# Kernel tuning notes

Hardware: AMD Instinct MI355X
Metric: run time of the kernel (lower is better)

Reference implementation:

```python
import jax, jax.numpy as jnp
import numpy as np

B, L, D, H, NL, V, W = 4, 2048, 512, 8, 4, 258, 8
HD = D // H


def setup_inputs() -> dict:
    key = jax.random.key(0)
    ks = jax.random.split(key, 12)
    s = 0.02
    x = jax.random.randint(ks[0], (B, L), 0, V, dtype=jnp.int32)
    patch_lengths = jnp.full((B, 256), W, dtype=jnp.int32)  # sum over patches == L
    emb = jax.random.normal(ks[1], (V, D), jnp.float32) * s
    ent_w = jax.random.normal(ks[2], (D, 1), jnp.float32) * s
    ent_b = jnp.zeros((D,), jnp.float32)
    qkv_w = jax.random.normal(ks[3], (NL, 3 * D, D), jnp.float32) * s
    qkv_b = jnp.zeros((NL, 3 * D), jnp.float32)
    ao_w = jax.random.normal(ks[4], (NL, D, D), jnp.float32) * s
    ao_b = jnp.zeros((NL, D), jnp.float32)
    ln1_s = jnp.ones((NL, D), jnp.float32)
    ln1_b = jnp.zeros((NL, D), jnp.float32)
    ln2_s = jnp.ones((NL, D), jnp.float32)
    ln2_b = jnp.zeros((NL, D), jnp.float32)
    ff1_w = jax.random.normal(ks[5], (NL, 4 * D, D), jnp.float32) * s
    ff1_b = jnp.zeros((NL, 4 * D), jnp.float32)
    ff2_w = jax.random.normal(ks[6], (NL, D, 4 * D), jnp.float32) * s
    ff2_b = jnp.zeros((NL, D), jnp.float32)
    out_w = jax.random.normal(ks[7], (V, D), jnp.float32) * s
    return {"emb": emb, "ent_w": ent_w, "ent_b": ent_b, "qkv_w": qkv_w,
            "qkv_b": qkv_b, "ao_w": ao_w, "ao_b": ao_b, "ln1_s": ln1_s,
            "ln1_b": ln1_b, "ln2_s": ln2_s, "ln2_b": ln2_b, "ff1_w": ff1_w,
            "ff1_b": ff1_b, "ff2_w": ff2_w, "ff2_b": ff2_b, "out_w": out_w,
            "x": x, "patch_lengths": patch_lengths}


def _layernorm(h, scale, bias, eps=1e-5):
    mu = jnp.mean(h, axis=-1, keepdims=True)
    var = jnp.mean(jnp.square(h - mu), axis=-1, keepdims=True)
    return (h - mu) * jax.lax.rsqrt(var + eps) * scale + bias


def _entropy_features(x, dtype):
    # fused sliding-window histogram via one-hot cumsum (replaces per-window bincount loop)
    onehot = jax.nn.one_hot(x, 256, dtype=dtype)            # [B, L, 256]
    c = jnp.cumsum(onehot, axis=1)
    cpad = jnp.concatenate([jnp.zeros_like(c[:, :1]), c], axis=1)
    counts = cpad[:, W:] - cpad[:, :-W]                     # [B, L-W+1, 256]
    p = counts / W
    ent = -jnp.sum(p * jnp.log2(p + 1e-10), axis=-1)        # zero-count terms contribute exactly 0
    full = jnp.zeros(x.shape, dtype).at[:, :x.shape[1] - W + 1].set(ent)
    return full[..., None]                                  # [B, L, 1]


def _block(h, p):
    qkv_w, qkv_b, ao_w, ao_b, l1s, l1b, l2s, l2b, f1w, f1b, f2w, f2b = p
    g = _layernorm(h, l1s, l1b)
    qkv = g @ qkv_w.T + qkv_b                                # [B, L, 3D]
    q, k, v = jnp.split(qkv, 3, axis=-1)
    q = q.reshape(B, L, H, HD)
    k = k.reshape(B, L, H, HD)
    v = v.reshape(B, L, H, HD)
    scores = jnp.einsum('blhd,bmhd->bhlm', q, k) / np.sqrt(HD).astype(h.dtype)
    attn = jax.nn.softmax(scores, axis=-1)
    o = jnp.einsum('bhlm,bmhd->blhd', attn, v).reshape(B, L, D)
    h = h + o @ ao_w.T + ao_b
    g = _layernorm(h, l2s, l2b)
    g = jax.nn.gelu(g @ f1w.T + f1b, approximate=False) @ f2w.T + f2b
    return h + g, None


def reference(emb, ent_w, ent_b, qkv_w, qkv_b, ao_w, ao_b, ln1_s, ln1_b,
              ln2_s, ln2_b, ff1_w, ff1_b, ff2_w, ff2_b, out_w, x, patch_lengths):
    tok = emb[x]                                             # [B, L, D]
    ent = _entropy_features(x, tok.dtype)                    # [B, L, 1]
    ent_emb = ent * ent_w[:, 0] + ent_b                      # Linear(1, D)
    h = tok + ent_emb
    h, _ = jax.lax.scan(_block, h,
                        (qkv_w, qkv_b, ao_w, ao_b, ln1_s, ln1_b,
                         ln2_s, ln2_b, ff1_w, ff1_b, ff2_w, ff2_b))
    # NOTE: the original module's global_transformer/patch-pool branch does not
    # feed the returned logits (dead code); logits come from the local stream h.
    logits = h @ out_w.T                                     # [B, L, V]
    return logits
```

## Files before the change

### kernel.cpp

```cpp
#include <hip/hip_runtime.h>
#include <hip/hip_bf16.h>
#include <math.h>

#define BB 4
#define LL 2048
#define DD 512
#define HH 8
#define NLAYER 4
#define VV 258
#define WW 8
#define HDIM 64
#define MM (BB * LL)
#define VPAD 384

#define C8 0.18033688f

typedef __attribute__((ext_vector_type(8))) short short8v;
typedef __attribute__((ext_vector_type(4))) float float4v;

typedef __attribute__((address_space(3))) unsigned int lds_u32;
typedef const __attribute__((address_space(1))) unsigned int glb_u32;

__device__ __forceinline__ unsigned short f2bf(float x) {
    unsigned int u = __float_as_uint(x);
    unsigned int r = (u + 0x7fffu + ((u >> 16) & 1u)) >> 16;
    return (unsigned short)r;
}
__device__ __forceinline__ float bf2f(unsigned short u) {
    return __uint_as_float((unsigned)u << 16);
}

__device__ __forceinline__ unsigned lds_addr(const void* p) {
    return (unsigned)(size_t)(__attribute__((address_space(3))) const void*)p;
}

#define E0 (NLAYER * 3 * DD * DD)
#define E1 (E0 + NLAYER * DD * DD)
#define E2 (E1 + NLAYER * 4 * DD * DD)
#define E3 (E2 + NLAYER * 4 * DD * DD)
#define E4 (E3 + VPAD * DD)

__global__ __launch_bounds__(256)
void cvt_all_kernel(const float* __restrict__ qkv_w, const float* __restrict__ ao_w,
                    const float* __restrict__ ff1_w, const float* __restrict__ ff2_w,
                    const float* __restrict__ out_w, unsigned short* __restrict__ dst)
{
    int i = (blockIdx.x * 256 + threadIdx.x) * 4;
    float4 v;
    if (i < E0)      v = *reinterpret_cast<const float4*>(qkv_w + i);
    else if (i < E1) v = *reinterpret_cast<const float4*>(ao_w + (i - E0));
    else if (i < E2) v = *reinterpret_cast<const float4*>(ff1_w + (i - E1));
    else if (i < E3) v = *reinterpret_cast<const float4*>(ff2_w + (i - E2));
    else {
        int idx = i - E3;
        if ((idx >> 9) < VV) v = *reinterpret_cast<const float4*>(out_w + idx);
        else                 v = (float4){0.f, 0.f, 0.f, 0.f};
    }
    uint2 pk;
    pk.x = (unsigned)f2bf(v.x) | ((unsigned)f2bf(v.y) << 16);
    pk.y = (unsigned)f2bf(v.z) | ((unsigned)f2bf(v.w) << 16);
    *reinterpret_cast<uint2*>(dst + i) = pk;
}

__global__ __launch_bounds__(256)
void embed_ln_kernel(const int* __restrict__ x,
                     const float* __restrict__ emb,
                     const float* __restrict__ ent_w,
                     const float* __restrict__ ent_b,
                     const float* __restrict__ ln_s,
                     const float* __restrict__ ln_b,
                     unsigned short* __restrict__ h,
                     unsigned short* __restrict__ g)
{
    int w = threadIdx.x >> 6, lane = threadIdx.x & 63;
    int row = blockIdx.x * 4 + w;
    int b = row / LL, l = row % LL;

    float ent = 0.f;
    if (l <= LL - WW) {
        int win[WW];
        #pragma unroll
        for (int i = 0; i < WW; i++) win[i] = x[b * LL + l + i];
        float s = 0.f;
        #pragma unroll
        for (int i = 0; i < WW; i++) {
            if (win[i] < 256) {
                int c = 0;
                #pragma unroll
                for (int j = 0; j < WW; j++) c += (win[j] == win[i]) ? 1 : 0;
                s += log2f((float)c * 0.125f + 1e-10f);
            }
        }
        ent = -s * 0.125f;
    }

    int tok = x[row];
    const float* erow = emb + (size_t)tok * DD + lane * 8;
    float v[8], ew[8], eb[8];
    *reinterpret_cast<float4*>(v)      = *reinterpret_cast<const float4*>(erow);
    *reinterpret_cast<float4*>(v + 4)  = *reinterpret_cast<const float4*>(erow + 4);
    *reinterpret_cast<float4*>(ew)     = *reinterpret_cast<const float4*>(ent_w + lane * 8);
    *reinterpret_cast<float4*>(ew + 4) = *reinterpret_cast<const float4*>(ent_w + lane * 8 + 4);
    *reinterpret_cast<float4*>(eb)     = *reinterpret_cast<const float4*>(ent_b + lane * 8);
    *reinterpret_cast<float4*>(eb + 4) = *reinterpret_cast<const float4*>(ent_b + lane * 8 + 4);

    float sum = 0.f, sq = 0.f;
    #pragma unroll
    for (int i = 0; i < 8; i++) {
        v[i] = v[i] + ent * ew[i] + eb[i];
        sum += v[i]; sq += v[i] * v[i];
    }
    unsigned int hpk[4];
    #pragma unroll
    for (int i = 0; i < 4; i++)
        hpk[i] = (unsigned)f2bf(v[2*i]) | ((unsigned)f2bf(v[2*i+1]) << 16);
    *reinterpret_cast<uint4*>(h + (size_t)row * DD + lane * 8) =
        *reinterpret_cast<const uint4*>(hpk);

    #pragma unroll
    for (int off = 32; off > 0; off >>= 1) {
        sum += __shfl_xor(sum, off);
        sq  += __shfl_xor(sq, off);
    }
    float mu = sum * (1.f / DD);
    float var = sq * (1.f / DD) - mu * mu;
    float rstd = rsqrtf(var + 1e-5f);

    float s8[8], bi[8];
    *reinterpret_cast<float4*>(s8)     = *reinterpret_cast<const float4*>(ln_s + lane * 8);
    *reinterpret_cast<float4*>(s8 + 4) = *reinterpret_cast<const float4*>(ln_s + lane * 8 + 4);
    *reinterpret_cast<float4*>(bi)     = *reinterpret_cast<const float4*>(ln_b + lane * 8);
    *reinterpret_cast<float4*>(bi + 4) = *reinterpret_cast<const float4*>(ln_b + lane * 8 + 4);

    unsigned int pk[4];
    #pragma unroll
    for (int i = 0; i < 4; i++) {
        unsigned short lo = f2bf((v[2*i]   - mu) * rstd * s8[2*i]   + bi[2*i]);
        unsigned short hi = f2bf((v[2*i+1] - mu) * rstd * s8[2*i+1] + bi[2*i+1]);
        pk[i] = (unsigned)lo | ((unsigned)hi << 16);
    }
    *reinterpret_cast<uint4*>(g + (size_t)row * DD + lane * 8) =
        *reinterpret_cast<const uint4*>(pk);
}

__global__ __launch_bounds__(256)
void ln_kernel(const unsigned short* __restrict__ h,
               const float* __restrict__ scale,
               const float* __restrict__ bias,
               unsigned short* __restrict__ g)
{
    int w = threadIdx.x >> 6, lane = threadIdx.x & 63;
    int row = blockIdx.x * 4 + w;

    uint4 raw = *reinterpret_cast<const uint4*>(h + (size_t)row * DD + lane * 8);
    const unsigned* rw = reinterpret_cast<const unsigned*>(&raw);
    float v[8];
    #pragma unroll
    for (int i = 0; i < 4; i++) {
        v[2*i]   = __uint_as_float(rw[i] << 16);
        v[2*i+1] = __uint_as_float(rw[i] & 0xffff0000u);
    }

    float sum = 0.f, sq = 0.f;
    #pragma unroll
    for (int i = 0; i < 8; i++) { sum += v[i]; sq += v[i] * v[i]; }
    #pragma unroll
    for (int off = 32; off > 0; off >>= 1) {
        sum += __shfl_xor(sum, off);
        sq  += __shfl_xor(sq, off);
    }
    float mu = sum * (1.f / DD);
    float var = sq * (1.f / DD) - mu * mu;
    float rstd = rsqrtf(var + 1e-5f);

    float s[8], bi[8];
    *reinterpret_cast<float4*>(s)      = *reinterpret_cast<const float4*>(scale + lane * 8);
    *reinterpret_cast<float4*>(s + 4)  = *reinterpret_cast<const float4*>(scale + lane * 8 + 4);
    *reinterpret_cast<float4*>(bi)     = *reinterpret_cast<const float4*>(bias + lane * 8);
    *reinterpret_cast<float4*>(bi + 4) = *reinterpret_cast<const float4*>(bias + lane * 8 + 4);

    unsigned int pk[4];
    #pragma unroll
    for (int i = 0; i < 4; i++) {
        unsigned short lo = f2bf((v[2*i]   - mu) * rstd * s[2*i]   + bi[2*i]);
        unsigned short hi = f2bf((v[2*i+1] - mu) * rstd * s[2*i+1] + bi[2*i+1]);
        pk[i] = (unsigned)lo | ((unsigned)hi << 16);
    }
    *reinterpret_cast<uint4*>(g + (size_t)row * DD + lane * 8) =
        *reinterpret_cast<const uint4*>(pk);
}

template<bool HAS_BIAS, bool GELU, bool RESID, int OMODE, int MT>
__global__ __launch_bounds__(MT * 2)
void gemm_mfma(const unsigned short* __restrict__ A,
               const unsigned short* __restrict__ W,
               const float* __restrict__ bias,
               const unsigned short* __restrict__ resid,
               void* __restrict__ Cv,
               int Nn, int Kk)
{
    constexpr int NW = MT / 32;
    constexpr int BLOADS = 512 / MT;
    constexpr int VMN = 4 + BLOADS;

    __shared__ unsigned short As[2][MT * 64];
    __shared__ unsigned short Bs[2][128 * 64];

    int t = threadIdx.x;
    int w = t >> 6, lane = t & 63;
    int wr = (MT == 128) ? (w >> 1) : 0;
    int wc = (MT == 128) ? (w & 1) : w;
    int l15 = lane & 15, l4 = lane >> 4;
    int m0 = blockIdx.y * MT, n0 = blockIdx.x * 128;

    int lrow = lane >> 3;
    int segp = (lane & 7) ^ lrow;

    float4v acc[4][4];
    #pragma unroll
    for (int i = 0; i < 4; i++)
        #pragma unroll
        for (int j = 0; j < 4; j++)
            acc[i][j] = (float4v){0.f, 0.f, 0.f, 0.f};

    #define STAGE(buf, k0) do {                                                   \
        _Pragma("unroll")                                                         \
        for (int i_ = 0; i_ < 4; i_++) {                                          \
            int r_ = i_ * (NW * 8) + w * 8 + lrow;                                \
            __builtin_amdgcn_global_load_lds(                                     \
                (glb_u32*)(A + (size_t)(m0 + r_) * Kk + (k0) + segp * 8),         \
                (lds_u32*)(As[buf] + i_ * (NW * 512) + w * 512), 16, 0, 0);       \
        }                                                                         \
        _Pragma("unroll")                                                         \
        for (int i_ = 0; i_ < BLOADS; i_++) {                                     \
            int r_ = i_ * (NW * 8) + w * 8 + lrow;                                \
            __builtin_amdgcn_global_load_lds(                                     \
                (glb_u32*)(W + (size_t)(n0 + r_) * Kk + (k0) + segp * 8),         \
                (lds_u32*)(Bs[buf] + i_ * (NW * 512) + w * 512), 16, 0, 0);       \
        } } while (0)

    int nk = Kk >> 6;
    STAGE(0, 0);
    for (int kt = 0; kt < nk; kt++) {
        int cur = kt & 1;
        if (kt + 1 < nk) {
            STAGE(cur ^ 1, (kt + 1) << 6);
            __builtin_amdgcn_sched_barrier(0);
            if constexpr (VMN == 8)  asm volatile("s_waitcnt vmcnt(8)");
            else                     asm volatile("s_waitcnt vmcnt(12)");
            __builtin_amdgcn_sched_barrier(0);
        } else {
            __builtin_amdgcn_sched_barrier(0);
            asm volatile("s_waitcnt vmcnt(0)");
            __builtin_amdgcn_sched_barrier(0);
        }
        __builtin_amdgcn_s_barrier();

        const char* asb = (const char*)As[cur];
        const char* bsb = (const char*)Bs[cur];
        #pragma unroll
        for (int kc = 0; kc < 2; kc++) {
            short8v af[4], bfr[4];
            #pragma unroll
            for (int mf = 0; mf < 4; mf++) {
                int row = wr * 64 + mf * 16 + l15;
                int off = (row * 128 + kc * 64 + l4 * 16) ^ ((row & 7) << 4);
                af[mf] = *reinterpret_cast<const short8v*>(asb + off);
            }
            #pragma unroll
            for (int nf = 0; nf < 4; nf++) {
                int row = wc * 64 + nf * 16 + l15;
                int off = (row * 128 + kc * 64 + l4 * 16) ^ ((row & 7) << 4);
                bfr[nf] = *reinterpret_cast<const short8v*>(bsb + off);
            }
            #pragma unroll
            for (int mf = 0; mf < 4; mf++)
                #pragma unroll
                for (int nf = 0; nf < 4; nf++)
                    acc[mf][nf] = __builtin_amdgcn_mfma_f32_16x16x32_bf16(
                        af[mf], bfr[nf], acc[mf][nf], 0, 0, 0);
        }
        __builtin_amdgcn_s_barrier();
    }
    #undef STAGE

    #pragma unroll
    for (int mf = 0; mf < 4; mf++)
        #pragma unroll
        for (int nf = 0; nf < 4; nf++)
            #pragma unroll
            for (int r = 0; r < 4; r++) {
                int m = m0 + wr * 64 + mf * 16 + l4 * 4 + r;
                int n = n0 + wc * 64 + nf * 16 + l15;
                if (n < Nn) {
                    float v = acc[mf][nf][r];
                    if (HAS_BIAS) v += bias[n];
                    if (GELU)     v = 0.5f * v * (1.f + erff(v * 0.70710678118654752f));
                    if (RESID)    v += bf2f(resid[(size_t)m * Nn + n]);
                    if (OMODE == 1)
                        ((unsigned short*)Cv)[(size_t)m * Nn + n] = f2bf(v);
                    else
                        ((float*)Cv)[(size_t)m * Nn + n] = v;
                }
            }
}

__global__ __launch_bounds__(512, 2)
void attn_mfma(const unsigned short* __restrict__ qkv, unsigned short* __restrict__ o)
{
    __shared__ unsigned short Kl[2][64 * 64];
    __shared__ unsigned short Vs[2][64 * 64];
    __shared__ unsigned short Pl[8 * 16 * 64];
    __shared__ float Scl[8][16];

    int t = threadIdx.x, w = t >> 6, lane = t & 63;
    int l15 = lane & 15, l4 = lane >> 4;

    int flat = blockIdx.x;
    int swz = (flat & 7) * 64 + (flat >> 3);
    int qt = swz & 15, hh = (swz >> 4) & 7, b = swz >> 7;

    int q0 = qt * 128 + w * 16;
    const int RS = 3 * DD;

    short8v qf[2];
    #pragma unroll
    for (int dh = 0; dh < 2; dh++) {
        size_t addr = (size_t)(b * LL + q0 + l15) * RS + hh * HDIM + dh * 32 + l4 * 8;
        qf[dh] = *reinterpret_cast<const short8v*>(qkv + addr);
    }

    float4v o_acc[4];
    #pragma unroll
    for (int dt = 0; dt < 4; dt++) o_acc[dt] = (float4v){0.f, 0.f, 0.f, 0.f};
    float l_run = 0.f;

    char* pbase = (char*)Pl + w * 2048;

    int lrow8 = lane >> 3;
    int ksegp = (lane & 7) ^ lrow8;
    int vrow = ((t >> 5) << 2) | ((t >> 1) & 3);
    int vseg = (((t >> 3) & 3) << 1) | (t & 1);
    const unsigned short* kgl = qkv + (size_t)(b * LL + w * 8 + lrow8) * RS
                              + hh * HDIM + DD + ksegp * 8;
    const unsigned short* vgl = qkv + (size_t)(b * LL + vrow) * RS
                              + hh * HDIM + 2 * DD + vseg * 8;
    const int step = 64 * RS;

    #define ASTAGE(buf) do {                                                      \
        __builtin_amdgcn_global_load_lds((glb_u32*)kgl,                           \
            (lds_u32*)(Kl[buf] + w * 512), 16, 0, 0);                             \
        __builtin_amdgcn_global_load_lds((glb_u32*)vgl,                           \
            (lds_u32*)(Vs[buf] + w * 512), 16, 0, 0);                             \
        kgl += step; vgl += step; } while (0)

    unsigned vtrbase = lds_addr(Vs) + ((lane >> 4) << 10)
                     + (((lane >> 2) & 3) << 5) + ((lane & 3) << 3);
    unsigned pswz = (unsigned)((l15 & 7) << 4);
    unsigned pa0 = lds_addr(pbase) + ((unsigned)(l15 * 128 + l4 * 16) ^ pswz);
    unsigned pa1 = lds_addr(pbase) + ((unsigned)(l15 * 128 + 64 + l4 * 16) ^ pswz);

    ASTAGE(0);
    asm volatile("s_waitcnt vmcnt(0)");
    __syncthreads();

    for (int kb = 0; kb < LL / 64; kb++) {
        int cur = kb & 1;
        if (kb + 1 < LL / 64) ASTAGE(cur ^ 1);

        const char* klc = (const char*)Kl[cur];
        unsigned vb = vtrbase + cur * 8192;

        float4v s_acc[4];
        __builtin_amdgcn_s_setprio(1);
        #pragma unroll
        for (int nt = 0; nt < 4; nt++) {
            s_acc[nt] = (float4v){0.f, 0.f, 0.f, 0.f};
            #pragma unroll
            for (int dh = 0; dh < 2; dh++) {
                int row = nt * 16 + l15;
                int off = (row * 128 + dh * 64 + l4 * 16) ^ ((row & 7) << 4);
                short8v kf = *reinterpret_cast<const short8v*>(klc + off);
                s_acc[nt] = __builtin_amdgcn_mfma_f32_16x16x32_bf16(kf, qf[dh], s_acc[nt], 0, 0, 0);
            }
        }
        __builtin_amdgcn_s_setprio(0);

        float ps = 0.f;
        #pragma unroll
        for (int nt = 0; nt < 4; nt++) {
            float p0 = __builtin_amdgcn_exp2f(s_acc[nt][0] * C8);
            float p1 = __builtin_amdgcn_exp2f(s_acc[nt][1] * C8);
            float p2 = __builtin_amdgcn_exp2f(s_acc[nt][2] * C8);
            float p3 = __builtin_amdgcn_exp2f(s_acc[nt][3] * C8);
            ps += (p0 + p1) + (p2 + p3);
            unsigned int pk0, pk1;
            asm("v_cvt_pk_bf16_f32 %0, %1, %2" : "=v"(pk0) : "v"(p0), "v"(p1));
            asm("v_cvt_pk_bf16_f32 %0, %1, %2" : "=v"(pk1) : "v"(p2), "v"(p3));
            uint2 pk; pk.x = pk0; pk.y = pk1;
            int off = (l15 * 128 + nt * 32 + l4 * 8) ^ ((l15 & 7) << 4);
            *reinterpret_cast<uint2*>(pbase + off) = pk;
        }
        l_run += ps;

        short8v pf0, pf1;
        asm volatile("ds_read_b128 %0, %1" : "=v"(pf0) : "v"(pa0) : "memory");
        asm volatile("ds_read_b128 %0, %1" : "=v"(pf1) : "v"(pa1) : "memory");
        unsigned long long a0, a1, a2, a3, a4, a5, a6, a7;
        unsigned long long b0, b1, b2, b3, b4, b5, b6, b7;
        unsigned ab0 = vb, ab1 = vb + 4096;
        asm volatile("ds_read_b64_tr_b16 %0, %1" : "=v"(a0) : "v"(ab0));
        asm volatile("ds_read_b64_tr_b16 %0, %1" : "=v"(a1) : "v"(ab0 + 512));
        asm volatile("ds_read_b64_tr_b16 %0, %1" : "=v"(a2) : "v"(ab0 + 128));
        asm volatile("ds_read_b64_tr_b16 %0, %1" : "=v"(a3) : "v"(ab0 + 640));
        asm volatile("ds_read_b64_tr_b16 %0, %1" : "=v"(a4) : "v"(ab0 + 256));
        asm volatile("ds_read_b64_tr_b16 %0, %1" : "=v"(a5) : "v"(ab0 + 768));
        asm volatile("ds_read_b64_tr_b16 %0, %1" : "=v"(a6) : "v"(ab0 + 384));
        asm volatile("ds_read_b64_tr_b16 %0, %1" : "=v"(a7) : "v"(ab0 + 896));
        asm volatile("ds_read_b64_tr_b16 %0, %1" : "=v"(b0) : "v"(ab1));
        asm volatile("ds_read_b64_tr_b16 %0, %1" : "=v"(b1) : "v"(ab1 + 512));
        asm volatile("ds_read_b64_tr_b16 %0, %1" : "=v"(b2) : "v"(ab1 + 128));
        asm volatile("ds_read_b64_tr_b16 %0, %1" : "=v"(b3) : "v"(ab1 + 640));
        asm volatile("ds_read_b64_tr_b16 %0, %1" : "=v"(b4) : "v"(ab1 + 256));
        asm volatile("ds_read_b64_tr_b16 %0, %1" : "=v"(b5) : "v"(ab1 + 768));
        asm volatile("ds_read_b64_tr_b16 %0, %1" : "=v"(b6) : "v"(ab1 + 384));
        asm volatile("ds_read_b64_tr_b16 %0, %1" : "=v"(b7) : "v"(ab1 + 896));
        union { unsigned long long q[2]; short8v v; } u0, u1, u2, u3;
        __builtin_amdgcn_s_setprio(1);
        asm volatile("s_waitcnt lgkmcnt(12)");
        __builtin_amdgcn_sched_barrier(0);
        u0.q[0] = a0; u0.q[1] = a1;
        u1.q[0] = a2; u1.q[1] = a3;
        o_acc[0] = __builtin_amdgcn_mfma_f32_16x16x32_bf16(pf0, u0.v, o_acc[0], 0, 0, 0);
        o_acc[1] = __builtin_amdgcn_mfma_f32_16x16x32_bf16(pf0, u1.v, o_acc[1], 0, 0, 0);
        asm volatile("s_waitcnt lgkmcnt(8)");
        __builtin_amdgcn_sched_barrier(0);
        u2.q[0] = a4; u2.q[1] = a5;
        u3.q[0] = a6; u3.q[1] = a7;
        o_acc[2] = __builtin_amdgcn_mfma_f32_16x16x32_bf16(pf0, u2.v, o_acc[2], 0, 0, 0);
        o_acc[3] = __builtin_amdgcn_mfma_f32_16x16x32_bf16(pf0, u3.v, o_acc[3], 0, 0, 0);
        asm volatile("s_waitcnt lgkmcnt(4)");
        __builtin_amdgcn_sched_barrier(0);
        u0.q[0] = b0; u0.q[1] = b1;
        u1.q[0] = b2; u1.q[1] = b3;
        o_acc[0] = __builtin_amdgcn_mfma_f32_16x16x32_bf16(pf1, u0.v, o_acc[0], 0, 0, 0);
        o_acc[1] = __builtin_amdgcn_mfma_f32_16x16x32_bf16(pf1, u1.v, o_acc[1], 0, 0, 0);
        asm volatile("s_waitcnt lgkmcnt(0)");
        __builtin_amdgcn_sched_barrier(0);
        u2.q[0] = b4; u2.q[1] = b5;
        u3.q[0] = b6; u3.q[1] = b7;
        o_acc[2] = __builtin_amdgcn_mfma_f32_16x16x32_bf16(pf1, u2.v, o_acc[2], 0, 0, 0);
        o_acc[3] = __builtin_amdgcn_mfma_f32_16x16x32_bf16(pf1, u3.v, o_acc[3], 0, 0, 0);
        __builtin_amdgcn_s_setprio(0);

        asm volatile("s_waitcnt vmcnt(0)");
        __syncthreads();
    }
    #undef ASTAGE

    float lt = l_run;
    lt += __shfl_xor(lt, 16);
    lt += __shfl_xor(lt, 32);
    if (l4 == 0) Scl[w][l15] = 1.f / lt;
    float4 iv = *reinterpret_cast<const float4*>(&Scl[w][l4 * 4]);
    float invs[4] = {iv.x, iv.y, iv.z, iv.w};
    #pragma unroll
    for (int r = 0; r < 4; r++) {
        int qg = q0 + l4 * 4 + r;
        #pragma unroll
        for (int dt = 0; dt < 4; dt++) {
            o[(size_t)(b * LL + qg) * DD + hh * HDIM + dt * 16 + l15] =
                f2bf(o_acc[dt][r] * invs[r]);
        }
    }
}

extern "C" void kernel_launch(void* const* d_in, const int* in_sizes, int n_in,
                              void* d_out, int out_size, void* d_ws, size_t ws_size,
                              hipStream_t stream)
{
    const float* emb    = (const float*)d_in[0];
    const float* ent_w  = (const float*)d_in[1];
    const float* ent_b  = (const float*)d_in[2];
    const float* qkv_w  = (const float*)d_in[3];
    const float* qkv_b  = (const float*)d_in[4];
    const float* ao_w   = (const float*)d_in[5];
    const float* ao_b   = (const float*)d_in[6];
    const float* ln1_s  = (const float*)d_in[7];
    const float* ln1_b  = (const float*)d_in[8];
    const float* ln2_s  = (const float*)d_in[9];
    const float* ln2_b  = (const float*)d_in[10];
    const float* ff1_w  = (const float*)d_in[11];
    const float* ff1_b  = (const float*)d_in[12];
    const float* ff2_w  = (const float*)d_in[13];
    const float* ff2_b  = (const float*)d_in[14];
    const float* out_w  = (const float*)d_in[15];
    const int*   x      = (const int*)d_in[16];

    float* out = (float*)d_out;

    const int NQW = NLAYER * 3 * DD * DD;
    const int NAW = NLAYER * DD * DD;
    const int NF1 = NLAYER * 4 * DD * DD;
    const int NF2 = NLAYER * DD * 4 * DD;

    char* p = (char*)d_ws;
    unsigned short* wq  = (unsigned short*)p; p += (size_t)NQW * 2;
    unsigned short* wa  = (unsigned short*)p; p += (size_t)NAW * 2;
    unsigned short* w1  = (unsigned short*)p; p += (size_t)NF1 * 2;
    unsigned short* w2  = (unsigned short*)p; p += (size_t)NF2 * 2;
    unsigned short* wob = (unsigned short*)p; p += (size_t)VPAD * DD * 2;
    unsigned short* h   = (unsigned short*)p; p += (size_t)MM * DD * 2;
    unsigned short* gb  = (unsigned short*)p; p += (size_t)MM * DD * 2;
    unsigned short* ob  = (unsigned short*)p; p += (size_t)MM * DD * 2;
    unsigned short* bb  = (unsigned short*)p; p += (size_t)MM * 4 * DD * 2;

    dim3 blk(256);

    cvt_all_kernel<<<E4 / 1024, blk, 0, stream>>>(qkv_w, ao_w, ff1_w, ff2_w, out_w, wq);

    embed_ln_kernel<<<MM / 4, blk, 0, stream>>>(x, emb, ent_w, ent_b,
                                                ln1_s, ln1_b, h, gb);

    for (int layer = 0; layer < NLAYER; layer++) {
        const unsigned short* qw = wq + (size_t)layer * 3 * DD * DD;
        const unsigned short* aw = wa + (size_t)layer * DD * DD;
        const unsigned short* f1 = w1 + (size_t)layer * 4 * DD * DD;
        const unsigned short* f2 = w2 + (size_t)layer * DD * 4 * DD;
        const float* qb  = qkv_b + (size_t)layer * 3 * DD;
        const float* ab  = ao_b  + (size_t)layer * DD;
        const float* l1s = ln1_s + (size_t)layer * DD;
        const float* l1b = ln1_b + (size_t)layer * DD;
        const float* l2s = ln2_s + (size_t)layer * DD;
        const float* l2b = ln2_b + (size_t)layer * DD;
        const float* f1b = ff1_b + (size_t)layer * 4 * DD;
        const float* f2b = ff2_b + (size_t)layer * DD;

        if (layer > 0)
            ln_kernel<<<MM / 4, blk, 0, stream>>>(h, l1s, l1b, gb);

        {
            dim3 grid((3 * DD) / 128, MM / 128);
            gemm_mfma<true, false, false, 1, 128><<<grid, 256, 0, stream>>>(
                gb, qw, qb, nullptr, bb, 3 * DD, DD);
        }

        attn_mfma<<<512, 512, 0, stream>>>(bb, ob);

        {
            dim3 grid(DD / 128, MM / 64);
            gemm_mfma<true, false, true, 1, 64><<<grid, 128, 0, stream>>>(
                ob, aw, ab, h, h, DD, DD);
        }

        ln_kernel<<<MM / 4, blk, 0, stream>>>(h, l2s, l2b, gb);

        {
            dim3 grid((4 * DD) / 128, MM / 128);
            gemm_mfma<true, true, false, 1, 128><<<grid, 256, 0, stream>>>(
                gb, f1, f1b, nullptr, bb, 4 * DD, DD);
        }

        {
            dim3 grid(DD / 128, MM / 64);
            gemm_mfma<true, false, true, 1, 64><<<grid, 128, 0, stream>>>(
                bb, f2, f2b, h, h, DD, 4 * DD);
        }
    }

    {
        dim3 grid(VPAD / 128, MM / 64);
        gemm_mfma<false, false, false, 0, 64><<<grid, 128, 0, stream>>>(
            h, wob, nullptr, nullptr, out, VV, DD);
    }
}
```

Before: 747.6 us.

## Keep attention probabilities in registers by permuting K rows; fold scale into QKV GEMM

The attention kernel no longer writes softmax probabilities to LDS and reads them back as MFMA operands. K rows are loaded in a permuted order so the S accumulator layout directly matches the A-operand layout of the PV MFMA, letting packed bf16 P values feed it from registers. The softmax scale constant is folded into the Q columns of the QKV GEMM epilogue, removing a multiply per score. This saves LDS traffic and waitcnts per key block, and rounding Q to bf16 after scaling changes numerics slightly.

```diff
diff --git a/kernel.cpp b/kernel.cpp
--- a/kernel.cpp
+++ b/kernel.cpp
@@ -190,7 +190,7 @@
         *reinterpret_cast<const uint4*>(pk);
 }
 
-template<bool HAS_BIAS, bool GELU, bool RESID, int OMODE, int MT>
+template<bool HAS_BIAS, bool GELU, bool RESID, bool QSCALE, int OMODE, int MT>
 __global__ __launch_bounds__(MT * 2)
 void gemm_mfma(const unsigned short* __restrict__ A,
                const unsigned short* __restrict__ W,
@@ -297,6 +297,7 @@
                     if (HAS_BIAS) v += bias[n];
                     if (GELU)     v = 0.5f * v * (1.f + erff(v * 0.70710678118654752f));
                     if (RESID)    v += bf2f(resid[(size_t)m * Nn + n]);
+                    if (QSCALE && n < DD) v *= C8;
                     if (OMODE == 1)
                         ((unsigned short*)Cv)[(size_t)m * Nn + n] = f2bf(v);
                     else
@@ -310,7 +311,6 @@
 {
     __shared__ unsigned short Kl[2][64 * 64];
     __shared__ unsigned short Vs[2][64 * 64];
-    __shared__ unsigned short Pl[8 * 16 * 64];
     __shared__ float Scl[8][16];
 
     int t = threadIdx.x, w = t >> 6, lane = t & 63;
@@ -335,13 +335,14 @@
     for (int dt = 0; dt < 4; dt++) o_acc[dt] = (float4v){0.f, 0.f, 0.f, 0.f};
     float l_run = 0.f;
 
-    char* pbase = (char*)Pl + w * 2048;
-
     int lrow8 = lane >> 3;
     int ksegp = (lane & 7) ^ lrow8;
+    int rho = w * 8 + lrow8;
+    int kappa = ((rho >> 5) << 5) | (((rho >> 4) & 1) << 2)
+              | (((rho >> 2) & 3) << 3) | (rho & 3);
     int vrow = ((t >> 5) << 2) | ((t >> 1) & 3);
     int vseg = (((t >> 3) & 3) << 1) | (t & 1);
-    const unsigned short* kgl = qkv + (size_t)(b * LL + w * 8 + lrow8) * RS
+    const unsigned short* kgl = qkv + (size_t)(b * LL + kappa) * RS
                               + hh * HDIM + DD + ksegp * 8;
     const unsigned short* vgl = qkv + (size_t)(b * LL + vrow) * RS
                               + hh * HDIM + 2 * DD + vseg * 8;
@@ -356,9 +357,6 @@
 
     unsigned vtrbase = lds_addr(Vs) + ((lane >> 4) << 10)
                      + (((lane >> 2) & 3) << 5) + ((lane & 3) << 3);
-    unsigned pswz = (unsigned)((l15 & 7) << 4);
-    unsigned pa0 = lds_addr(pbase) + ((unsigned)(l15 * 128 + l4 * 16) ^ pswz);
-    unsigned pa1 = lds_addr(pbase) + ((unsigned)(l15 * 128 + 64 + l4 * 16) ^ pswz);
 
     ASTAGE(0);
     asm volatile("s_waitcnt vmcnt(0)");
@@ -386,26 +384,6 @@
         }
         __builtin_amdgcn_s_setprio(0);
 
-        float ps = 0.f;
-        #pragma unroll
-        for (int nt = 0; nt < 4; nt++) {
-            float p0 = __builtin_amdgcn_exp2f(s_acc[nt][0] * C8);
-            float p1 = __builtin_amdgcn_exp2f(s_acc[nt][1] * C8);
-            float p2 = __builtin_amdgcn_exp2f(s_acc[nt][2] * C8);
-            float p3 = __builtin_amdgcn_exp2f(s_acc[nt][3] * C8);
-            ps += (p0 + p1) + (p2 + p3);
-            unsigned int pk0, pk1;
-            asm("v_cvt_pk_bf16_f32 %0, %1, %2" : "=v"(pk0) : "v"(p0), "v"(p1));
-            asm("v_cvt_pk_bf16_f32 %0, %1, %2" : "=v"(pk1) : "v"(p2), "v"(p3));
-            uint2 pk; pk.x = pk0; pk.y = pk1;
-            int off = (l15 * 128 + nt * 32 + l4 * 8) ^ ((l15 & 7) << 4);
-            *reinterpret_cast<uint2*>(pbase + off) = pk;
-        }
-        l_run += ps;
-
-        short8v pf0, pf1;
-        asm volatile("ds_read_b128 %0, %1" : "=v"(pf0) : "v"(pa0) : "memory");
-        asm volatile("ds_read_b128 %0, %1" : "=v"(pf1) : "v"(pa1) : "memory");
         unsigned long long a0, a1, a2, a3, a4, a5, a6, a7;
         unsigned long long b0, b1, b2, b3, b4, b5, b6, b7;
         unsigned ab0 = vb, ab1 = vb + 4096;
@@ -425,32 +403,65 @@
         asm volatile("ds_read_b64_tr_b16 %0, %1" : "=v"(b5) : "v"(ab1 + 768));
         asm volatile("ds_read_b64_tr_b16 %0, %1" : "=v"(b6) : "v"(ab1 + 384));
         asm volatile("ds_read_b64_tr_b16 %0, %1" : "=v"(b7) : "v"(ab1 + 896));
+
+        union { unsigned u[4]; short8v v; } pf0u, pf1u;
+        float ps;
+        {
+            float p0 = __builtin_amdgcn_exp2f(s_acc[0][0]);
+            float p1 = __builtin_amdgcn_exp2f(s_acc[0][1]);
+            float p2 = __builtin_amdgcn_exp2f(s_acc[0][2]);
+            float p3 = __builtin_amdgcn_exp2f(s_acc[0][3]);
+            float p4 = __builtin_amdgcn_exp2f(s_acc[1][0]);
+            float p5 = __builtin_amdgcn_exp2f(s_acc[1][1]);
+            float p6 = __builtin_amdgcn_exp2f(s_acc[1][2]);
+            float p7 = __builtin_amdgcn_exp2f(s_acc[1][3]);
+            asm("v_cvt_pk_bf16_f32 %0, %1, %2" : "=v"(pf0u.u[0]) : "v"(p0), "v"(p1));
+            asm("v_cvt_pk_bf16_f32 %0, %1, %2" : "=v"(pf0u.u[1]) : "v"(p2), "v"(p3));
+            asm("v_cvt_pk_bf16_f32 %0, %1, %2" : "=v"(pf0u.u[2]) : "v"(p4), "v"(p5));
+            asm("v_cvt_pk_bf16_f32 %0, %1, %2" : "=v"(pf0u.u[3]) : "v"(p6), "v"(p7));
+            ps = ((p0 + p1) + (p2 + p3)) + ((p4 + p5) + (p6 + p7));
+        }
+        {
+            float p0 = __builtin_amdgcn_exp2f(s_acc[2][0]);
+            float p1 = __builtin_amdgcn_exp2f(s_acc[2][1]);
+            float p2 = __builtin_amdgcn_exp2f(s_acc[2][2]);
+            float p3 = __builtin_amdgcn_exp2f(s_acc[2][3]);
+            float p4 = __builtin_amdgcn_exp2f(s_acc[3][0]);
+            float p5 = __builtin_amdgcn_exp2f(s_acc[3][1]);
+            float p6 = __builtin_amdgcn_exp2f(s_acc[3][2]);
+            float p7 = __builtin_amdgcn_exp2f(s_acc[3][3]);
+            asm("v_cvt_pk_bf16_f32 %0, %1, %2" : "=v"(pf1u.u[0]) : "v"(p0), "v"(p1));
+            asm("v_cvt_pk_bf16_f32 %0, %1, %2" : "=v"(pf1u.u[1]) : "v"(p2), "v"(p3));
+            asm("v_cvt_pk_bf16_f32 %0, %1, %2" : "=v"(pf1u.u[2]) : "v"(p4), "v"(p5));
+            asm("v_cvt_pk_bf16_f32 %0, %1, %2" : "=v"(pf1u.u[3]) : "v"(p6), "v"(p7));
+            ps += ((p0 + p1) + (p2 + p3)) + ((p4 + p5) + (p6 + p7));
+        }
+        l_run += ps;
+
         union { unsigned long long q[2]; short8v v; } u0, u1, u2, u3;
+        asm volatile("s_waitcnt lgkmcnt(8)");
+        __builtin_amdgcn_sched_barrier(0);
         __builtin_amdgcn_s_setprio(1);
-        asm volatile("s_waitcnt lgkmcnt(12)");
-        __builtin_amdgcn_sched_barrier(0);
         u0.q[0] = a0; u0.q[1] = a1;
         u1.q[0] = a2; u1.q[1] = a3;
-        o_acc[0] = __builtin_amdgcn_mfma_f32_16x16x32_bf16(pf0, u0.v, o_acc[0], 0, 0, 0);
-        o_acc[1] = __builtin_amdgcn_mfma_f32_16x16x32_bf16(pf0, u1.v, o_acc[1], 0, 0, 0);
-        asm volatile("s_waitcnt lgkmcnt(8)");
+        o_acc[0] = __builtin_amdgcn_mfma_f32_16x16x32_bf16(pf0u.v, u0.v, o_acc[0], 0, 0, 0);
+        o_acc[1] = __builtin_amdgcn_mfma_f32_16x16x32_bf16(pf0u.v, u1.v, o_acc[1], 0, 0, 0);
+        asm volatile("s_waitcnt lgkmcnt(4)");
         __builtin_amdgcn_sched_barrier(0);
         u2.q[0] = a4; u2.q[1] = a5;
         u3.q[0] = a6; u3.q[1] = a7;
-        o_acc[2] = __builtin_amdgcn_mfma_f32_16x16x32_bf16(pf0, u2.v, o_acc[2], 0, 0, 0);
-        o_acc[3] = __builtin_amdgcn_mfma_f32_16x16x32_bf16(pf0, u3.v, o_acc[3], 0, 0, 0);
-        asm volatile("s_waitcnt lgkmcnt(4)");
+        o_acc[2] = __builtin_amdgcn_mfma_f32_16x16x32_bf16(pf0u.v, u2.v, o_acc[2], 0, 0, 0);
+        o_acc[3] = __builtin_amdgcn_mfma_f32_16x16x32_bf16(pf0u.v, u3.v, o_acc[3], 0, 0, 0);
+        asm volatile("s_waitcnt lgkmcnt(0)");
         __builtin_amdgcn_sched_barrier(0);
         u0.q[0] = b0; u0.q[1] = b1;
         u1.q[0] = b2; u1.q[1] = b3;
-        o_acc[0] = __builtin_amdgcn_mfma_f32_16x16x32_bf16(pf1, u0.v, o_acc[0], 0, 0, 0);
-        o_acc[1] = __builtin_amdgcn_mfma_f32_16x16x32_bf16(pf1, u1.v, o_acc[1], 0, 0, 0);
-        asm volatile("s_waitcnt lgkmcnt(0)");
-        __builtin_amdgcn_sched_barrier(0);
         u2.q[0] = b4; u2.q[1] = b5;
         u3.q[0] = b6; u3.q[1] = b7;
-        o_acc[2] = __builtin_amdgcn_mfma_f32_16x16x32_bf16(pf1, u2.v, o_acc[2], 0, 0, 0);
-        o_acc[3] = __builtin_amdgcn_mfma_f32_16x16x32_bf16(pf1, u3.v, o_acc[3], 0, 0, 0);
+        o_acc[0] = __builtin_amdgcn_mfma_f32_16x16x32_bf16(pf1u.v, u0.v, o_acc[0], 0, 0, 0);
+        o_acc[1] = __builtin_amdgcn_mfma_f32_16x16x32_bf16(pf1u.v, u1.v, o_acc[1], 0, 0, 0);
+        o_acc[2] = __builtin_amdgcn_mfma_f32_16x16x32_bf16(pf1u.v, u2.v, o_acc[2], 0, 0, 0);
+        o_acc[3] = __builtin_amdgcn_mfma_f32_16x16x32_bf16(pf1u.v, u3.v, o_acc[3], 0, 0, 0);
         __builtin_amdgcn_s_setprio(0);
 
         asm volatile("s_waitcnt vmcnt(0)");
@@ -541,7 +552,7 @@
 
         {
             dim3 grid((3 * DD) / 128, MM / 128);
-            gemm_mfma<true, false, false, 1, 128><<<grid, 256, 0, stream>>>(
+            gemm_mfma<true, false, false, true, 1, 128><<<grid, 256, 0, stream>>>(
                 gb, qw, qb, nullptr, bb, 3 * DD, DD);
         }
 
@@ -549,7 +560,7 @@
 
         {
             dim3 grid(DD / 128, MM / 64);
-            gemm_mfma<true, false, true, 1, 64><<<grid, 128, 0, stream>>>(
+            gemm_mfma<true, false, true, false, 1, 64><<<grid, 128, 0, stream>>>(
                 ob, aw, ab, h, h, DD, DD);
         }
 
@@ -557,20 +568,20 @@
 
         {
             dim3 grid((4 * DD) / 128, MM / 128);
-            gemm_mfma<true, true, false, 1, 128><<<grid, 256, 0, stream>>>(
+            gemm_mfma<true, true, false, false, 1, 128><<<grid, 256, 0, stream>>>(
                 gb, f1, f1b, nullptr, bb, 4 * DD, DD);
         }
 
         {
             dim3 grid(DD / 128, MM / 64);
-            gemm_mfma<true, false, true, 1, 64><<<grid, 128, 0, stream>>>(
+            gemm_mfma<true, false, true, false, 1, 64><<<grid, 128, 0, stream>>>(
                 bb, f2, f2b, h, h, DD, 4 * DD);
         }
     }
 
     {
         dim3 grid(VPAD / 128, MM / 64);
-        gemm_mfma<false, false, false, 0, 64><<<grid, 128, 0, stream>>>(
+        gemm_mfma<false, false, false, false, 0, 64><<<grid, 128, 0, stream>>>(
             h, wob, nullptr, nullptr, out, VV, DD);
     }
 }
```

After: 718.0 us. 1.04x faster.
